# Optimization experiments

Hardware: AMD Instinct MI355X
Metric: run time of the kernel (lower is better)

## Reference

```python
import jax, jax.numpy as jnp
import numpy as np

B, LQ, LK, QD, KD, VD, H = 8, 128, 1024, 128, 128, 128, 128
NEG_INF = -1e6  # d2l masked_softmax fill value


def setup_inputs() -> dict:
    key = jax.random.key(0)
    k1, k2, k3, k4, k5, k6, k7 = jax.random.split(key, 7)
    return {
        "queries": jax.random.normal(k1, (B, LQ, QD), dtype=jnp.float32),
        "keys": jax.random.normal(k2, (B, LK, KD), dtype=jnp.float32),
        "values": jax.random.normal(k3, (B, LK, VD), dtype=jnp.float32),
        "valid_lens": jax.random.randint(k4, (B,), 0, LK),
        # learned params: torch Linear(in,out,bias=False); stored here as [in,out]
        "W_q": jax.random.normal(k5, (QD, H), dtype=jnp.float32) / np.sqrt(QD),
        "W_k": jax.random.normal(k6, (KD, H), dtype=jnp.float32) / np.sqrt(KD),
        "w_v": jax.random.normal(k7, (H,), dtype=jnp.float32) / np.sqrt(H),
    }


def reference(queries, keys, values, valid_lens, W_q, W_k, w_v):
    q = jnp.einsum("blq,qh->blh", queries, W_q)            # [B,Lq,H]
    k = jnp.einsum("bsk,kh->bsh", keys, W_k)               # [B,Lk,H]
    features = jnp.tanh(q[:, :, None, :] + k[:, None, :, :])  # [B,Lq,Lk,H]
    scores = jnp.einsum("blsh,h->bls", features, w_v)      # [B,Lq,Lk]
    mask = jnp.arange(LK)[None, None, :] < valid_lens[:, None, None]
    scores = jnp.where(mask, scores, NEG_INF)
    attn = jax.nn.softmax(scores, axis=-1)                 # dropout p=0.0 -> identity
    return jnp.einsum("bls,bsv->blv", attn, values)        # [B,Lq,Vd]
```

## Files before the change

### kernel.cpp

```cpp
#include <hip/hip_runtime.h>
#include <hip/hip_fp16.h>

#define B_   8
#define LQ_  128
#define LK_  1024
#define H_   128

__device__ float        g_eq  [B_ * LQ_ * H_];
__device__ unsigned int g_ekT2[B_ * H_ * (LK_ / 2)];

#define C2LOG2E 2.8853900817779268f

__global__ __launch_bounds__(256) void proj_kernel(const float* __restrict__ q,
                                                   const float* __restrict__ k,
                                                   const float* __restrict__ Wq,
                                                   const float* __restrict__ Wk) {
    __shared__ float Ws[H_ * 64];
    __shared__ float Xs[32 * H_];
    const int t = threadIdx.x;
    const int tile = blockIdx.x;
    const int ch = blockIdx.y;
    const bool isq = (tile < 32);
    const float* X; const float* W; int r0;
    if (isq) { X = q; W = Wq; r0 = tile * 32; }
    else     { X = k; W = Wk; r0 = (tile - 32) * 32; }

    #pragma unroll
    for (int u = 0; u < 8; ++u) {
        int p = u * 256 + t;
        int kk = p >> 4, c4 = p & 15;
        *(float4*)(Ws + kk * 64 + c4 * 4) = *(const float4*)(W + kk * H_ + ch * 64 + c4 * 4);
    }
    #pragma unroll
    for (int u = 0; u < 4; ++u) {
        int idx = u * 256 + t;
        int r = idx >> 5, c = idx & 31;
        *(float4*)(Xs + r * H_ + c * 4) = *(const float4*)(X + (size_t)(r0 + r) * H_ + c * 4);
    }
    __syncthreads();

    const int r4 = t >> 5;
    const int tc = t & 31;
    float acc[4][2] = {};
    #pragma unroll 4
    for (int kk = 0; kk < H_; ++kk) {
        float2 w2 = *(const float2*)(Ws + kk * 64 + tc * 2);
        #pragma unroll
        for (int i = 0; i < 4; ++i) {
            float x = Xs[(r4 * 4 + i) * H_ + kk];
            acc[i][0] = fmaf(x, w2.x, acc[i][0]);
            acc[i][1] = fmaf(x, w2.y, acc[i][1]);
        }
    }
    if (isq) {
        #pragma unroll
        for (int i = 0; i < 4; ++i) {
            float2 o;
            o.x = __builtin_amdgcn_exp2f(acc[i][0] * C2LOG2E);
            o.y = __builtin_amdgcn_exp2f(acc[i][1] * C2LOG2E);
            *(float2*)(g_eq + (size_t)(r0 + r4 * 4 + i) * H_ + ch * 64 + tc * 2) = o;
        }
    } else {
        const int b = r0 >> 10;
        const int sb = (r0 & 1023) + r4 * 4;
        #pragma unroll
        for (int j = 0; j < 2; ++j) {
            const int h = ch * 64 + tc * 2 + j;
            float e0 = __builtin_amdgcn_exp2f(acc[0][j] * C2LOG2E);
            float e1 = __builtin_amdgcn_exp2f(acc[1][j] * C2LOG2E);
            float e2 = __builtin_amdgcn_exp2f(acc[2][j] * C2LOG2E);
            float e3 = __builtin_amdgcn_exp2f(acc[3][j] * C2LOG2E);
            __half2 p0 = __floats2half2_rn(e0, e1);
            __half2 p1 = __floats2half2_rn(e2, e3);
            uint2 pk = make_uint2(*(unsigned int*)&p0, *(unsigned int*)&p1);
            *(uint2*)(g_ekT2 + (size_t)(b * H_ + h) * (LK_ / 2) + (sb >> 1)) = pk;
        }
    }
}

__global__ __launch_bounds__(512) void fused_attn(const float* __restrict__ values,
                                                  const int* __restrict__ valid_lens,
                                                  const float* __restrict__ w_v,
                                                  float* __restrict__ out) {
    __shared__ float sA[LK_], sB[LK_];
    __shared__ float red[8], sred[16];
    __shared__ float rinvs[2];
    __shared__ float part[8][2][H_];
    const int t = threadIdx.x;
    const int b = blockIdx.x >> 6, l0 = (blockIdx.x & 63) * 2;
    int valid = valid_lens[b];
    valid = min(max(valid, 0), LK_);

    const int s0 = 2 * t;
    if (s0 < valid) {
        const float* __restrict__ q0 = g_eq + (size_t)(b * LQ_ + l0) * H_;
        const float* __restrict__ q1 = q0 + H_;
        const unsigned int* __restrict__ ek = g_ekT2 + (size_t)b * H_ * (LK_ / 2) + t;
        float a00 = 0.0f, a01 = 0.0f, a10 = 0.0f, a11 = 0.0f, wsum = 0.0f;
        #pragma unroll 4
        for (int h = 0; h < H_; ++h) {
            unsigned int u = ek[(size_t)h * (LK_ / 2)];
            float2 ef = __half22float2(*(const __half2*)&u);
            const float e0 = ef.x, e1 = ef.y;
            const float qa = q0[h], qb = q1[h], wh = w_v[h];
            wsum += wh;
            a00 = fmaf(wh, __builtin_amdgcn_rcpf(fmaf(qa, e0, 1.0f)), a00);
            a01 = fmaf(wh, __builtin_amdgcn_rcpf(fmaf(qa, e1, 1.0f)), a01);
            a10 = fmaf(wh, __builtin_amdgcn_rcpf(fmaf(qb, e0, 1.0f)), a10);
            a11 = fmaf(wh, __builtin_amdgcn_rcpf(fmaf(qb, e1, 1.0f)), a11);
        }
        *(float2*)(sA + s0) = make_float2(fmaf(-2.0f, a00, wsum), fmaf(-2.0f, a01, wsum));
        *(float2*)(sB + s0) = make_float2(fmaf(-2.0f, a10, wsum), fmaf(-2.0f, a11, wsum));
    }
    __syncthreads();

    int n;
    if (valid == 0) {
        n = LK_;
        for (int i = t; i < LK_; i += 512) { sA[i] = 1.0f; sB[i] = 1.0f; }
        if (t == 0) { rinvs[0] = 1.0f / 1024.0f; rinvs[1] = 1.0f / 1024.0f; }
    } else {
        n = valid;
        const int r = t >> 8, tt = t & 255;
        const int w4id = tt >> 6;
        float* srow = r ? sB : sA;
        float m = -3.0e38f;
        for (int i = tt; i < n; i += 256) m = fmaxf(m, srow[i]);
        #pragma unroll
        for (int kk = 32; kk; kk >>= 1) m = fmaxf(m, __shfl_xor(m, kk, 64));
        if ((tt & 63) == 0) red[r * 4 + w4id] = m;
        __syncthreads();
        m = fmaxf(fmaxf(red[r * 4], red[r * 4 + 1]), fmaxf(red[r * 4 + 2], red[r * 4 + 3]));
        float ps = 0.0f;
        for (int i = tt; i < n; i += 256) {
            float e = __builtin_amdgcn_exp2f((srow[i] - m) * 1.44269504f);
            srow[i] = e;
            ps += e;
        }
        #pragma unroll
        for (int kk = 32; kk; kk >>= 1) ps += __shfl_xor(ps, kk, 64);
        if ((tt & 63) == 0) sred[r * 4 + w4id] = ps;
        __syncthreads();
        if (t < 2) {
            float s4 = (sred[t * 4] + sred[t * 4 + 1]) + (sred[t * 4 + 2] + sred[t * 4 + 3]);
            rinvs[t] = 1.0f / s4;
        }
    }
    __syncthreads();

    const int c = t >> 6;
    const int v2 = t & 63;
    const float* vb = values + (size_t)b * LK_ * H_ + 2 * v2;
    float ax0 = 0.0f, ay0 = 0.0f, ax1 = 0.0f, ay1 = 0.0f;
    #pragma unroll 4
    for (int s = c; s < n; s += 8) {
        float2 vv = *(const float2*)(vb + (size_t)s * H_);
        float w0 = sA[s], w1 = sB[s];
        ax0 = fmaf(w0, vv.x, ax0); ay0 = fmaf(w0, vv.y, ay0);
        ax1 = fmaf(w1, vv.x, ax1); ay1 = fmaf(w1, vv.y, ay1);
    }
    *(float2*)(&part[c][0][2 * v2]) = make_float2(ax0, ay0);
    *(float2*)(&part[c][1][2 * v2]) = make_float2(ax1, ay1);
    __syncthreads();
    if (t < 256) {
        const int l = t >> 7, v = t & 127;
        float o = (((part[0][l][v] + part[1][l][v]) + (part[2][l][v] + part[3][l][v]))
                 + ((part[4][l][v] + part[5][l][v]) + (part[6][l][v] + part[7][l][v])));
        out[(b * LQ_ + l0 + l) * H_ + v] = o * rinvs[l];
    }
}

extern "C" void kernel_launch(void* const* d_in, const int* in_sizes, int n_in,
                              void* d_out, int out_size, void* d_ws, size_t ws_size,
                              hipStream_t stream) {
    const float* queries    = (const float*)d_in[0];
    const float* keys       = (const float*)d_in[1];
    const float* values     = (const float*)d_in[2];
    const int*   valid_lens = (const int*)d_in[3];
    const float* W_q        = (const float*)d_in[4];
    const float* W_k        = (const float*)d_in[5];
    const float* w_v        = (const float*)d_in[6];
    float* out = (float*)d_out;
    (void)d_ws; (void)ws_size; (void)in_sizes; (void)n_in; (void)out_size;

    proj_kernel<<<dim3(288, 2), 256, 0, stream>>>(queries, keys, W_q, W_k);
    fused_attn <<<512, 512, 0, stream>>>(values, valid_lens, w_v, out);
}
```

Before: 41.04 us.

## Process four query rows per block in fused attention to reuse keys and values

Each fused_attn block now handles four query rows instead of two, and the grid is halved to 256 blocks. Each fp16 key-exponent load and each value load is reused across four rows, which cuts global traffic per score and per output. In exchange, each thread holds more registers and shared memory grows, and with only 256 blocks on a large GPU occupancy and parallelism drop.

```diff
diff --git a/kernel.cpp b/kernel.cpp
--- a/kernel.cpp
+++ b/kernel.cpp
@@ -82,91 +82,96 @@
                                                   const int* __restrict__ valid_lens,
                                                   const float* __restrict__ w_v,
                                                   float* __restrict__ out) {
-    __shared__ float sA[LK_], sB[LK_];
-    __shared__ float red[8], sred[16];
-    __shared__ float rinvs[2];
-    __shared__ float part[8][2][H_];
+    __shared__ float sc[4][LK_];
+    __shared__ float red[8], sred[8];
+    __shared__ float rinvs[4];
+    __shared__ float part[8][4][H_];
     const int t = threadIdx.x;
-    const int b = blockIdx.x >> 6, l0 = (blockIdx.x & 63) * 2;
+    const int b = blockIdx.x >> 5, l0 = (blockIdx.x & 31) * 4;
     int valid = valid_lens[b];
     valid = min(max(valid, 0), LK_);
 
     const int s0 = 2 * t;
     if (s0 < valid) {
-        const float* __restrict__ q0 = g_eq + (size_t)(b * LQ_ + l0) * H_;
-        const float* __restrict__ q1 = q0 + H_;
+        const float* __restrict__ qr = g_eq + (size_t)(b * LQ_ + l0) * H_;
         const unsigned int* __restrict__ ek = g_ekT2 + (size_t)b * H_ * (LK_ / 2) + t;
-        float a00 = 0.0f, a01 = 0.0f, a10 = 0.0f, a11 = 0.0f, wsum = 0.0f;
-        #pragma unroll 4
+        float a[4][2] = {};
+        float wsum = 0.0f;
+        #pragma unroll 2
         for (int h = 0; h < H_; ++h) {
             unsigned int u = ek[(size_t)h * (LK_ / 2)];
             float2 ef = __half22float2(*(const __half2*)&u);
-            const float e0 = ef.x, e1 = ef.y;
-            const float qa = q0[h], qb = q1[h], wh = w_v[h];
+            const float wh = w_v[h];
             wsum += wh;
-            a00 = fmaf(wh, __builtin_amdgcn_rcpf(fmaf(qa, e0, 1.0f)), a00);
-            a01 = fmaf(wh, __builtin_amdgcn_rcpf(fmaf(qa, e1, 1.0f)), a01);
-            a10 = fmaf(wh, __builtin_amdgcn_rcpf(fmaf(qb, e0, 1.0f)), a10);
-            a11 = fmaf(wh, __builtin_amdgcn_rcpf(fmaf(qb, e1, 1.0f)), a11);
+            #pragma unroll
+            for (int r = 0; r < 4; ++r) {
+                const float qh = qr[r * H_ + h];
+                a[r][0] = fmaf(wh, __builtin_amdgcn_rcpf(fmaf(qh, ef.x, 1.0f)), a[r][0]);
+                a[r][1] = fmaf(wh, __builtin_amdgcn_rcpf(fmaf(qh, ef.y, 1.0f)), a[r][1]);
+            }
         }
-        *(float2*)(sA + s0) = make_float2(fmaf(-2.0f, a00, wsum), fmaf(-2.0f, a01, wsum));
-        *(float2*)(sB + s0) = make_float2(fmaf(-2.0f, a10, wsum), fmaf(-2.0f, a11, wsum));
+        #pragma unroll
+        for (int r = 0; r < 4; ++r)
+            *(float2*)(&sc[r][s0]) = make_float2(fmaf(-2.0f, a[r][0], wsum),
+                                                 fmaf(-2.0f, a[r][1], wsum));
     }
     __syncthreads();
 
     int n;
     if (valid == 0) {
         n = LK_;
-        for (int i = t; i < LK_; i += 512) { sA[i] = 1.0f; sB[i] = 1.0f; }
-        if (t == 0) { rinvs[0] = 1.0f / 1024.0f; rinvs[1] = 1.0f / 1024.0f; }
+        for (int i = t; i < 4 * LK_; i += 512) sc[i >> 10][i & 1023] = 1.0f;
+        if (t < 4) rinvs[t] = 1.0f / 1024.0f;
     } else {
         n = valid;
-        const int r = t >> 8, tt = t & 255;
-        const int w4id = tt >> 6;
-        float* srow = r ? sB : sA;
+        const int r = t >> 7;
+        const int tt = t & 127;
+        const int wid = (t >> 6) & 1;
+        float* srow = sc[r];
         float m = -3.0e38f;
-        for (int i = tt; i < n; i += 256) m = fmaxf(m, srow[i]);
+        for (int i = tt; i < n; i += 128) m = fmaxf(m, srow[i]);
         #pragma unroll
         for (int kk = 32; kk; kk >>= 1) m = fmaxf(m, __shfl_xor(m, kk, 64));
-        if ((tt & 63) == 0) red[r * 4 + w4id] = m;
+        if ((tt & 63) == 0) red[r * 2 + wid] = m;
         __syncthreads();
-        m = fmaxf(fmaxf(red[r * 4], red[r * 4 + 1]), fmaxf(red[r * 4 + 2], red[r * 4 + 3]));
+        m = fmaxf(red[r * 2], red[r * 2 + 1]);
         float ps = 0.0f;
-        for (int i = tt; i < n; i += 256) {
+        for (int i = tt; i < n; i += 128) {
             float e = __builtin_amdgcn_exp2f((srow[i] - m) * 1.44269504f);
             srow[i] = e;
             ps += e;
         }
         #pragma unroll
         for (int kk = 32; kk; kk >>= 1) ps += __shfl_xor(ps, kk, 64);
-        if ((tt & 63) == 0) sred[r * 4 + w4id] = ps;
+        if ((tt & 63) == 0) sred[r * 2 + wid] = ps;
         __syncthreads();
-        if (t < 2) {
-            float s4 = (sred[t * 4] + sred[t * 4 + 1]) + (sred[t * 4 + 2] + sred[t * 4 + 3]);
-            rinvs[t] = 1.0f / s4;
-        }
+        if (t < 4) rinvs[t] = 1.0f / (sred[t * 2] + sred[t * 2 + 1]);
     }
     __syncthreads();
 
     const int c = t >> 6;
     const int v2 = t & 63;
     const float* vb = values + (size_t)b * LK_ * H_ + 2 * v2;
-    float ax0 = 0.0f, ay0 = 0.0f, ax1 = 0.0f, ay1 = 0.0f;
+    float ax[4] = {}, ay[4] = {};
     #pragma unroll 4
     for (int s = c; s < n; s += 8) {
         float2 vv = *(const float2*)(vb + (size_t)s * H_);
-        float w0 = sA[s], w1 = sB[s];
-        ax0 = fmaf(w0, vv.x, ax0); ay0 = fmaf(w0, vv.y, ay0);
-        ax1 = fmaf(w1, vv.x, ax1); ay1 = fmaf(w1, vv.y, ay1);
+        #pragma unroll
+        for (int r = 0; r < 4; ++r) {
+            float w = sc[r][s];
+            ax[r] = fmaf(w, vv.x, ax[r]);
+            ay[r] = fmaf(w, vv.y, ay[r]);
+        }
     }
-    *(float2*)(&part[c][0][2 * v2]) = make_float2(ax0, ay0);
-    *(float2*)(&part[c][1][2 * v2]) = make_float2(ax1, ay1);
+    #pragma unroll
+    for (int r = 0; r < 4; ++r)
+        *(float2*)(&part[c][r][2 * v2]) = make_float2(ax[r], ay[r]);
     __syncthreads();
-    if (t < 256) {
-        const int l = t >> 7, v = t & 127;
-        float o = (((part[0][l][v] + part[1][l][v]) + (part[2][l][v] + part[3][l][v]))
-                 + ((part[4][l][v] + part[5][l][v]) + (part[6][l][v] + part[7][l][v])));
-        out[(b * LQ_ + l0 + l) * H_ + v] = o * rinvs[l];
+    {
+        const int rr = t >> 7, v = t & 127;
+        float o = (((part[0][rr][v] + part[1][rr][v]) + (part[2][rr][v] + part[3][rr][v]))
+                 + ((part[4][rr][v] + part[5][rr][v]) + (part[6][rr][v] + part[7][rr][v])));
+        out[(b * LQ_ + l0 + rr) * H_ + v] = o * rinvs[rr];
     }
 }
 
@@ -184,5 +189,5 @@
     (void)d_ws; (void)ws_size; (void)in_sizes; (void)n_in; (void)out_size;
 
     proj_kernel<<<dim3(288, 2), 256, 0, stream>>>(queries, keys, W_q, W_k);
-    fused_attn <<<512, 512, 0, stream>>>(values, valid_lens, w_v, out);
+    fused_attn <<<256, 512, 0, stream>>>(values, valid_lens, w_v, out);
 }
```

Result: slower. 51.04 us (+24.4%).

## Convert values to fp16 in a pre-pass and software-prefetch ekT loads

Applied to the files above, without the earlier changes.

Adds a separate kernel that converts the values tensor to packed fp16, so the attention-weighted sum in fused_attn reads half the bytes per element. It also rewrites the score loop to software-prefetch the next four ekT rows into registers while computing on the current four. The extra launch reads all of values once and writes an fp16 copy, which may cost more than the read traffic it saves. fp16 values also reduce output precision.

```diff
diff --git a/kernel.cpp b/kernel.cpp
--- a/kernel.cpp
+++ b/kernel.cpp
@@ -8,6 +8,7 @@
 
 __device__ float        g_eq  [B_ * LQ_ * H_];
 __device__ unsigned int g_ekT2[B_ * H_ * (LK_ / 2)];
+__device__ unsigned int g_vh  [B_ * LK_ * (H_ / 2)];
 
 #define C2LOG2E 2.8853900817779268f
 
@@ -78,8 +79,15 @@
     }
 }
 
-__global__ __launch_bounds__(512) void fused_attn(const float* __restrict__ values,
-                                                  const int* __restrict__ valid_lens,
+__global__ __launch_bounds__(256) void conv_values(const float* __restrict__ values) {
+    const int idx = blockIdx.x * 256 + threadIdx.x;
+    float4 v = *(const float4*)(values + (size_t)idx * 4);
+    __half2 p0 = __floats2half2_rn(v.x, v.y);
+    __half2 p1 = __floats2half2_rn(v.z, v.w);
+    *(uint2*)(g_vh + (size_t)idx * 2) = make_uint2(*(unsigned int*)&p0, *(unsigned int*)&p1);
+}
+
+__global__ __launch_bounds__(512) void fused_attn(const int* __restrict__ valid_lens,
                                                   const float* __restrict__ w_v,
                                                   float* __restrict__ out) {
     __shared__ float sA[LK_], sB[LK_];
@@ -97,17 +105,30 @@
         const float* __restrict__ q1 = q0 + H_;
         const unsigned int* __restrict__ ek = g_ekT2 + (size_t)b * H_ * (LK_ / 2) + t;
         float a00 = 0.0f, a01 = 0.0f, a10 = 0.0f, a11 = 0.0f, wsum = 0.0f;
-        #pragma unroll 4
-        for (int h = 0; h < H_; ++h) {
-            unsigned int u = ek[(size_t)h * (LK_ / 2)];
-            float2 ef = __half22float2(*(const __half2*)&u);
-            const float e0 = ef.x, e1 = ef.y;
-            const float qa = q0[h], qb = q1[h], wh = w_v[h];
-            wsum += wh;
-            a00 = fmaf(wh, __builtin_amdgcn_rcpf(fmaf(qa, e0, 1.0f)), a00);
-            a01 = fmaf(wh, __builtin_amdgcn_rcpf(fmaf(qa, e1, 1.0f)), a01);
-            a10 = fmaf(wh, __builtin_amdgcn_rcpf(fmaf(qb, e0, 1.0f)), a10);
-            a11 = fmaf(wh, __builtin_amdgcn_rcpf(fmaf(qb, e1, 1.0f)), a11);
+        unsigned int pf0 = ek[0 * (LK_ / 2)];
+        unsigned int pf1 = ek[1 * (LK_ / 2)];
+        unsigned int pf2 = ek[2 * (LK_ / 2)];
+        unsigned int pf3 = ek[3 * (LK_ / 2)];
+        for (int h0 = 0; h0 < H_; h0 += 4) {
+            const unsigned int c0 = pf0, c1 = pf1, c2 = pf2, c3 = pf3;
+            if (h0 + 8 <= H_) {
+                pf0 = ek[(size_t)(h0 + 4) * (LK_ / 2)];
+                pf1 = ek[(size_t)(h0 + 5) * (LK_ / 2)];
+                pf2 = ek[(size_t)(h0 + 6) * (LK_ / 2)];
+                pf3 = ek[(size_t)(h0 + 7) * (LK_ / 2)];
+            }
+            #pragma unroll
+            for (int i = 0; i < 4; ++i) {
+                const unsigned int u = (i == 0) ? c0 : (i == 1) ? c1 : (i == 2) ? c2 : c3;
+                float2 ef = __half22float2(*(const __half2*)&u);
+                const int h = h0 + i;
+                const float qa = q0[h], qb = q1[h], wh = w_v[h];
+                wsum += wh;
+                a00 = fmaf(wh, __builtin_amdgcn_rcpf(fmaf(qa, ef.x, 1.0f)), a00);
+                a01 = fmaf(wh, __builtin_amdgcn_rcpf(fmaf(qa, ef.y, 1.0f)), a01);
+                a10 = fmaf(wh, __builtin_amdgcn_rcpf(fmaf(qb, ef.x, 1.0f)), a10);
+                a11 = fmaf(wh, __builtin_amdgcn_rcpf(fmaf(qb, ef.y, 1.0f)), a11);
+            }
         }
         *(float2*)(sA + s0) = make_float2(fmaf(-2.0f, a00, wsum), fmaf(-2.0f, a01, wsum));
         *(float2*)(sB + s0) = make_float2(fmaf(-2.0f, a10, wsum), fmaf(-2.0f, a11, wsum));
@@ -150,11 +171,12 @@
 
     const int c = t >> 6;
     const int v2 = t & 63;
-    const float* vb = values + (size_t)b * LK_ * H_ + 2 * v2;
+    const unsigned int* vb = g_vh + (size_t)b * LK_ * (H_ / 2) + v2;
     float ax0 = 0.0f, ay0 = 0.0f, ax1 = 0.0f, ay1 = 0.0f;
     #pragma unroll 4
     for (int s = c; s < n; s += 8) {
-        float2 vv = *(const float2*)(vb + (size_t)s * H_);
+        unsigned int u = vb[(size_t)s * (H_ / 2)];
+        float2 vv = __half22float2(*(const __half2*)&u);
         float w0 = sA[s], w1 = sB[s];
         ax0 = fmaf(w0, vv.x, ax0); ay0 = fmaf(w0, vv.y, ay0);
         ax1 = fmaf(w1, vv.x, ax1); ay1 = fmaf(w1, vv.y, ay1);
@@ -184,5 +206,6 @@
     (void)d_ws; (void)ws_size; (void)in_sizes; (void)n_in; (void)out_size;
 
     proj_kernel<<<dim3(288, 2), 256, 0, stream>>>(queries, keys, W_q, W_k);
-    fused_attn <<<512, 512, 0, stream>>>(values, valid_lens, w_v, out);
-}
+    conv_values<<<1024, 256, 0, stream>>>(values);
+    fused_attn <<<512, 512, 0, stream>>>(valid_lens, w_v, out);
+}
```

Result: slower. 45.68 us (+11.3%).
